# Optimization experiments

Hardware: AMD Instinct MI355X
Metric: run time of the kernel (lower is better)

## Reference

```python
import jax, jax.numpy as jnp
from jax import lax
import numpy as np

B, T, C = 32, 2048, 512
CLAMP_LO, CLAMP_HI = 1e-4, 1.0 - 1e-4


def setup_inputs() -> dict:
    key = jax.random.key(0)
    x = jax.random.normal(key, (B, T, C), dtype=jnp.float32)
    # parameter initialized at logit(0.9), repeated per channel
    logit_alpha = jnp.full((C,), float(np.log(0.9 / 0.1)), dtype=jnp.float32)
    delta = jnp.asarray(1.0, dtype=jnp.float32)
    return {"x": x, "logit_alpha": logit_alpha, "delta": delta}


def reference(x, logit_alpha, delta):
    # x: [B, T, C]; logit_alpha: [C]; delta: scalar
    a = jnp.clip(jax.nn.sigmoid(logit_alpha), CLAMP_LO, CLAMP_HI).astype(x.dtype)  # [C]
    one_minus_a = 1.0 - a  # [C], broadcasts over [B, C]
    d = delta.astype(x.dtype)

    def step(y_prev, x_t):  # y_prev, x_t: [B, C]
        r = x_t - y_prev
        g = jnp.where(jnp.abs(r) <= d, r, d * jnp.sign(r))  # Huber gradient
        y = y_prev + one_minus_a * g
        return y, y

    y0 = x[:, 0, :]  # [B, C]
    xs = jnp.swapaxes(x[:, 1:, :], 0, 1)  # [T-1, B, C]
    _, ys = lax.scan(step, y0, xs)  # ys: [T-1, B, C]
    y = jnp.concatenate([y0[None], ys], axis=0)  # [T, B, C]
    return jnp.swapaxes(y, 0, 1)  # [B, T, C]
```

## Files before the change

### kernel.cpp

```cpp
#include <hip/hip_runtime.h>
#include <math.h>


#define TT   2048
#define CC   512
#define TILE 32
#define NTIL (TT / TILE)
#define LPT  8
#define RING 4

__device__ __forceinline__ void async16(const float* g, float* l) {
    __builtin_amdgcn_global_load_lds(
        (const __attribute__((address_space(1))) void*)g,
        (__attribute__((address_space(3))) void*)l, 16, 0, 0);
}

template<int N> __device__ __forceinline__ void vm_wait() {
    if constexpr (N == 24) asm volatile("s_waitcnt vmcnt(24)" ::: "memory");
    else if constexpr (N == 32) asm volatile("s_waitcnt vmcnt(32)" ::: "memory");
    else if constexpr (N == 40) asm volatile("s_waitcnt vmcnt(40)" ::: "memory");
    else if constexpr (N == 48) asm volatile("s_waitcnt vmcnt(48)" ::: "memory");
    else                        asm volatile("s_waitcnt vmcnt(0)"  ::: "memory");
    __builtin_amdgcn_sched_barrier(0);
}

template<int WAITN, bool PF>
__device__ __forceinline__ void tile_body(int k, const float* __restrict__ xl,
                                          float* __restrict__ yl,
                                          float* __restrict__ xslot,
                                          float* __restrict__ ysb,
                                          float& yv, float oma, float d, int lane)
{
    vm_wait<WAITN>();

    float xin[TILE];
    #pragma unroll
    for (int i = 0; i < TILE; ++i) xin[i] = xslot[i * 64 + lane];
    __builtin_amdgcn_sched_barrier(0);

    #pragma unroll
    for (int i = 0; i < TILE; ++i) {
        float r = xin[i] - yv;
        yv += oma * fminf(fmaxf(r, -d), d);
        ysb[i * 64 + lane] = yv;
    }
    __builtin_amdgcn_sched_barrier(0);

    #pragma unroll
    for (int g = 0; g < LPT; ++g) {
        float4 v = *(const float4*)&ysb[g * 256 + (lane << 2)];
        *(float4*)(yl + (size_t)(k * TILE + g * 4) * CC) = v;
    }
    __builtin_amdgcn_sched_barrier(0);

    if (PF) {
        #pragma unroll
        for (int g = 0; g < LPT; ++g)
            async16(xl + (size_t)((k + RING) * TILE + g * 4) * CC,
                    &xslot[g * 256]);
    }
    __builtin_amdgcn_sched_barrier(0);
}

__global__ __launch_bounds__(64, 1)
void huber_ema_kernel(const float* __restrict__ x,
                      const float* __restrict__ logit_alpha,
                      const float* __restrict__ delta,
                      float* __restrict__ y)
{
    const int blk  = blockIdx.x;
    const int b    = blk >> 3;
    const int cc   = blk & 7;
    const int lane = threadIdx.x;

    __shared__ float xs[RING][TILE * 64];
    __shared__ float ys[TILE * 64];

    const float la = logit_alpha[(cc << 6) + lane];
    const float d  = delta[0];
    const float* __restrict__ xb = x + (size_t)b * TT * CC + (cc << 6);
    float*       __restrict__ yb = y + (size_t)b * TT * CC + (cc << 6);
    float yv = xb[lane];

    float a = 1.0f / (1.0f + expf(-la));
    a = fminf(fmaxf(a, 1e-4f), 1.0f - 1e-4f);
    const float oma = 1.0f - a;

    const float* __restrict__ xl = xb + (size_t)(lane >> 4) * CC + ((lane & 15) << 2);
    float*       __restrict__ yl = yb + (size_t)(lane >> 4) * CC + ((lane & 15) << 2);

    #pragma unroll
    for (int t = 0; t < RING; ++t) {
        #pragma unroll
        for (int g = 0; g < LPT; ++g)
            async16(xl + (size_t)(t * TILE + g * 4) * CC, &xs[t][g * 256]);
    }

    tile_body<24, true >(0, xl, yl, xs[0], ys, yv, oma, d, lane);
    tile_body<32, true >(1, xl, yl, xs[1], ys, yv, oma, d, lane);
    tile_body<40, true >(2, xl, yl, xs[2], ys, yv, oma, d, lane);

    for (int k = 3; k <= NTIL - 5; ++k)
        tile_body<48, true >(k, xl, yl, xs[k & 3], ys, yv, oma, d, lane);

    tile_body<48, false>(NTIL - 4, xl, yl, xs[(NTIL - 4) & 3], ys, yv, oma, d, lane);
    tile_body<40, false>(NTIL - 3, xl, yl, xs[(NTIL - 3) & 3], ys, yv, oma, d, lane);
    tile_body<32, false>(NTIL - 2, xl, yl, xs[(NTIL - 2) & 3], ys, yv, oma, d, lane);
    tile_body<24, false>(NTIL - 1, xl, yl, xs[(NTIL - 1) & 3], ys, yv, oma, d, lane);
}

extern "C" void kernel_launch(void* const* d_in, const int* in_sizes, int n_in,
                              void* d_out, int out_size, void* d_ws, size_t ws_size,
                              hipStream_t stream) {
    const float* x  = (const float*)d_in[0];
    const float* la = (const float*)d_in[1];
    const float* dl = (const float*)d_in[2];
    float* y = (float*)d_out;

    huber_ema_kernel<<<dim3(256), dim3(64), 0, stream>>>(x, la, dl, y);
}
```

Before: 271.3 us.

## Warp-specialize scan into loader, compute, and storer wavefronts

Splits the single-wavefront kernel into three wavefronts: one issues async global-to-LDS loads three tiles ahead, one runs the serial Huber-EMA recurrence, and one writes the previous tile's results to global memory from a double-buffered LDS staging area. The goal is to take load issue and store traffic off the critical serial dependency chain. In exchange, every tile now needs a block-wide barrier, and the prefetch depth drops from four tiles ahead to three.

```diff
diff --git a/kernel.cpp b/kernel.cpp
--- a/kernel.cpp
+++ b/kernel.cpp
@@ -16,53 +16,24 @@
 }
 
 template<int N> __device__ __forceinline__ void vm_wait() {
-    if constexpr (N == 24) asm volatile("s_waitcnt vmcnt(24)" ::: "memory");
-    else if constexpr (N == 32) asm volatile("s_waitcnt vmcnt(32)" ::: "memory");
-    else if constexpr (N == 40) asm volatile("s_waitcnt vmcnt(40)" ::: "memory");
-    else if constexpr (N == 48) asm volatile("s_waitcnt vmcnt(48)" ::: "memory");
-    else                        asm volatile("s_waitcnt vmcnt(0)"  ::: "memory");
+    if constexpr (N == 0)  asm volatile("s_waitcnt vmcnt(0)"  ::: "memory");
+    else if constexpr (N == 8)  asm volatile("s_waitcnt vmcnt(8)"  ::: "memory");
+    else if constexpr (N == 16) asm volatile("s_waitcnt vmcnt(16)" ::: "memory");
     __builtin_amdgcn_sched_barrier(0);
 }
 
-template<int WAITN, bool PF>
-__device__ __forceinline__ void tile_body(int k, const float* __restrict__ xl,
-                                          float* __restrict__ yl,
-                                          float* __restrict__ xslot,
-                                          float* __restrict__ ysb,
-                                          float& yv, float oma, float d, int lane)
-{
-    vm_wait<WAITN>();
-
-    float xin[TILE];
-    #pragma unroll
-    for (int i = 0; i < TILE; ++i) xin[i] = xslot[i * 64 + lane];
-    __builtin_amdgcn_sched_barrier(0);
-
-    #pragma unroll
-    for (int i = 0; i < TILE; ++i) {
-        float r = xin[i] - yv;
-        yv += oma * fminf(fmaxf(r, -d), d);
-        ysb[i * 64 + lane] = yv;
-    }
-    __builtin_amdgcn_sched_barrier(0);
-
-    #pragma unroll
-    for (int g = 0; g < LPT; ++g) {
-        float4 v = *(const float4*)&ysb[g * 256 + (lane << 2)];
-        *(float4*)(yl + (size_t)(k * TILE + g * 4) * CC) = v;
-    }
-    __builtin_amdgcn_sched_barrier(0);
-
-    if (PF) {
-        #pragma unroll
-        for (int g = 0; g < LPT; ++g)
-            async16(xl + (size_t)((k + RING) * TILE + g * 4) * CC,
-                    &xslot[g * 256]);
-    }
+__device__ __forceinline__ void lgkm0() {
+    asm volatile("s_waitcnt lgkmcnt(0)" ::: "memory");
     __builtin_amdgcn_sched_barrier(0);
 }
 
-__global__ __launch_bounds__(64, 1)
+__device__ __forceinline__ void bar() {
+    __builtin_amdgcn_sched_barrier(0);
+    __builtin_amdgcn_s_barrier();
+    __builtin_amdgcn_sched_barrier(0);
+}
+
+__global__ __launch_bounds__(192, 1)
 void huber_ema_kernel(const float* __restrict__ x,
                       const float* __restrict__ logit_alpha,
                       const float* __restrict__ delta,
@@ -71,42 +42,85 @@
     const int blk  = blockIdx.x;
     const int b    = blk >> 3;
     const int cc   = blk & 7;
-    const int lane = threadIdx.x;
+    const int tid  = threadIdx.x;
+    const int lane = tid & 63;
+    const int wid  = tid >> 6;
 
     __shared__ float xs[RING][TILE * 64];
-    __shared__ float ys[TILE * 64];
+    __shared__ float ys[2][TILE * 64];
 
-    const float la = logit_alpha[(cc << 6) + lane];
-    const float d  = delta[0];
     const float* __restrict__ xb = x + (size_t)b * TT * CC + (cc << 6);
     float*       __restrict__ yb = y + (size_t)b * TT * CC + (cc << 6);
-    float yv = xb[lane];
-
-    float a = 1.0f / (1.0f + expf(-la));
-    a = fminf(fmaxf(a, 1e-4f), 1.0f - 1e-4f);
-    const float oma = 1.0f - a;
-
     const float* __restrict__ xl = xb + (size_t)(lane >> 4) * CC + ((lane & 15) << 2);
     float*       __restrict__ yl = yb + (size_t)(lane >> 4) * CC + ((lane & 15) << 2);
 
-    #pragma unroll
-    for (int t = 0; t < RING; ++t) {
+    float yv = 0.f, oma = 0.f, d = 0.f;
+
+    if (wid == 0) {
         #pragma unroll
-        for (int g = 0; g < LPT; ++g)
-            async16(xl + (size_t)(t * TILE + g * 4) * CC, &xs[t][g * 256]);
+        for (int t = 0; t < 3; ++t) {
+            #pragma unroll
+            for (int g = 0; g < LPT; ++g)
+                async16(xl + (size_t)(t * TILE + g * 4) * CC, &xs[t][g * 256]);
+        }
+        vm_wait<16>();
+    } else if (wid == 1) {
+        const float la = logit_alpha[(cc << 6) + lane];
+        d  = delta[0];
+        yv = xb[lane];
+        float a = 1.0f / (1.0f + expf(-la));
+        a = fminf(fmaxf(a, 1e-4f), 1.0f - 1e-4f);
+        oma = 1.0f - a;
+    }
+    bar();
+
+    for (int k = 0; k < NTIL; ++k) {
+        if (wid == 0) {
+            if (k + 3 < NTIL) {
+                #pragma unroll
+                for (int g = 0; g < LPT; ++g)
+                    async16(xl + (size_t)((k + 3) * TILE + g * 4) * CC,
+                            &xs[(k + 3) & (RING - 1)][g * 256]);
+                vm_wait<16>();
+            } else if (k == NTIL - 3) { vm_wait<8>(); }
+            else if (k == NTIL - 2)   { vm_wait<0>(); }
+        } else if (wid == 1) {
+            const float* __restrict__ bx = xs[k & (RING - 1)];
+            float*       __restrict__ by = ys[k & 1];
+            float xin[TILE];
+            #pragma unroll
+            for (int i = 0; i < TILE; ++i) xin[i] = bx[i * 64 + lane];
+            __builtin_amdgcn_sched_barrier(0);
+            #pragma unroll
+            for (int i = 0; i < TILE; ++i) {
+                float r = xin[i] - yv;
+                yv += oma * fminf(fmaxf(r, -d), d);
+                by[i * 64 + lane] = yv;
+            }
+            lgkm0();
+        } else {
+            if (k > 0) {
+                const float* __restrict__ sy = ys[(k - 1) & 1];
+                const size_t tb = (size_t)(k - 1) * TILE;
+                #pragma unroll
+                for (int g = 0; g < LPT; ++g) {
+                    float4 v = *(const float4*)&sy[g * 256 + (lane << 2)];
+                    *(float4*)(yl + (tb + (size_t)(g * 4)) * CC) = v;
+                }
+            }
+        }
+        bar();
     }
 
-    tile_body<24, true >(0, xl, yl, xs[0], ys, yv, oma, d, lane);
-    tile_body<32, true >(1, xl, yl, xs[1], ys, yv, oma, d, lane);
-    tile_body<40, true >(2, xl, yl, xs[2], ys, yv, oma, d, lane);
-
-    for (int k = 3; k <= NTIL - 5; ++k)
-        tile_body<48, true >(k, xl, yl, xs[k & 3], ys, yv, oma, d, lane);
-
-    tile_body<48, false>(NTIL - 4, xl, yl, xs[(NTIL - 4) & 3], ys, yv, oma, d, lane);
-    tile_body<40, false>(NTIL - 3, xl, yl, xs[(NTIL - 3) & 3], ys, yv, oma, d, lane);
-    tile_body<32, false>(NTIL - 2, xl, yl, xs[(NTIL - 2) & 3], ys, yv, oma, d, lane);
-    tile_body<24, false>(NTIL - 1, xl, yl, xs[(NTIL - 1) & 3], ys, yv, oma, d, lane);
+    if (wid == 2) {
+        const float* __restrict__ sy = ys[(NTIL - 1) & 1];
+        const size_t tb = (size_t)(NTIL - 1) * TILE;
+        #pragma unroll
+        for (int g = 0; g < LPT; ++g) {
+            float4 v = *(const float4*)&sy[g * 256 + (lane << 2)];
+            *(float4*)(yl + (tb + (size_t)(g * 4)) * CC) = v;
+        }
+    }
 }
 
 extern "C" void kernel_launch(void* const* d_in, const int* in_sizes, int n_in,
@@ -117,5 +131,5 @@
     const float* dl = (const float*)d_in[2];
     float* y = (float*)d_out;
 
-    huber_ema_kernel<<<dim3(256), dim3(64), 0, stream>>>(x, la, dl, y);
+    huber_ema_kernel<<<dim3(256), dim3(192), 0, stream>>>(x, la, dl, y);
 }
```

Result: faster. 246.4 us (-9.2%).
